# Kernel optimization log

Measured on AMD Instinct MI355X. Metric: run time of the kernel, lower is better.

## Reference

```python
import jax, jax.numpy as jnp
import numpy as np

N, D, E, R, EJ = 100000, 128, 600000, 200, 300000


def setup_inputs() -> dict:
    key = jax.random.key(0)
    ks = jax.random.split(key, 14)
    s = 1.0 / np.sqrt(D)
    return {
        "emb": jax.random.normal(ks[0], (N, D), jnp.float32),
        "change": jax.random.normal(ks[1], (N, D), jnp.float32),
        "W1": jax.random.normal(ks[2], (D, D), jnp.float32) * s,
        "Wloop1": jax.random.normal(ks[3], (D, D), jnp.float32) * s,
        "rel_emb1": jax.random.normal(ks[4], (R, D), jnp.float32),
        "W2": jax.random.normal(ks[5], (D, D), jnp.float32) * s,
        "Wloop2": jax.random.normal(ks[6], (D, D), jnp.float32) * s,
        "rel_emb2": jax.random.normal(ks[7], (R, D), jnp.float32),
        "res": jnp.array([0.1], jnp.float32),
        "jump_weight": jnp.array([1.0], jnp.float32),
        "edge_w_jump": jax.random.uniform(ks[8], (EJ,), jnp.float32),
        "edge_index": jax.random.randint(ks[9], (2, E), 0, N, jnp.int32),
        "edge_type": jax.random.randint(ks[10], (E,), 0, R, jnp.int32),
        "edge_id_jump": jax.random.randint(ks[11], (2, EJ), 0, N, jnp.int32),
    }


def _mgcn_conv(x, W, Wloop, rel_emb, edge_index, edge_type, num_e):
    # Relational (CompGCN-style mult composition) conv: gather-compose-scatter.
    src, dst = edge_index[0], edge_index[1]
    msg = x[src] * rel_emb[edge_type]                      # [E, D]
    agg = jax.ops.segment_sum(msg, dst, num_segments=num_e)
    deg = jax.ops.segment_sum(jnp.ones(src.shape, x.dtype), dst, num_segments=num_e)
    agg = agg / jnp.maximum(deg, 1.0)[:, None]
    return jnp.tanh(agg @ W + x @ Wloop)


def reference(emb, change, W1, Wloop1, rel_emb1, W2, Wloop2, rel_emb2, res,
              jump_weight, edge_w_jump, edge_index, edge_type, edge_id_jump):
    num_e = emb.shape[0]
    jump_emb = emb
    # residual-scaled two-layer relational GCN (dropout = identity in eval)
    h = emb + res[0] * _mgcn_conv(emb, W1, Wloop1, rel_emb1, edge_index, edge_type, num_e)
    h = h + res[0] * _mgcn_conv(h, W2, Wloop2, rel_emb2, edge_index, edge_type, num_e)
    # jump diffusion: weighted scatter over jump edge list
    jsrc, jdst = edge_id_jump[0], edge_id_jump[1]
    jump_res = jax.ops.segment_sum(edge_w_jump[:, None] * jump_emb[jsrc], jdst,
                                   num_segments=num_e)
    dchange = h + jump_weight[0] * jump_res
    return (change, dchange)
```

## Files before the change

kernel.cpp:

```cpp
#include <hip/hip_runtime.h>
#include <math.h>

#define D 128

typedef __attribute__((ext_vector_type(8))) short short8v;
typedef __attribute__((ext_vector_type(4))) float f32x4;
typedef _Float16 half2n __attribute__((ext_vector_type(2)));
typedef _Float16 half8v __attribute__((ext_vector_type(8)));

__device__ inline short f2h(float f) {
    _Float16 h = (_Float16)f;
    return __builtin_bit_cast(short, h);
}
__device__ inline float h2f(short s) {
    return (float)__builtin_bit_cast(_Float16, s);
}
__device__ inline unsigned char h2e5(short hs) {
    unsigned u = (unsigned short)hs;
    u = u + 0x7Fu + ((u >> 8) & 1u);
    return (unsigned char)(u >> 8);
}
__device__ inline half2n u2h2(unsigned u) { return __builtin_bit_cast(half2n, u); }
__device__ inline unsigned h22u(half2n h) { return __builtin_bit_cast(unsigned, h); }

__device__ inline float fast_tanh(float x) {
    float a = fabsf(x);
    float e = __expf(-2.0f * a);
    float t = (1.0f - e) / (1.0f + e);
    return copysignf(t, x);
}

__device__ inline void e5fma(uint2 xw, uint4 rw,
                             half2n& a0, half2n& a1, half2n& a2, half2n& a3) {
    a0 += u2h2(xw.x & 0xFF00FF00u) * u2h2(rw.x);
    a1 += u2h2((xw.x << 8) & 0xFF00FF00u) * u2h2(rw.y);
    a2 += u2h2(xw.y & 0xFF00FF00u) * u2h2(rw.z);
    a3 += u2h2((xw.y << 8) & 0xFF00FF00u) * u2h2(rw.w);
}
__device__ inline void h16fma(uint4 xw, half2n w2,
                              half2n& a0, half2n& a1, half2n& a2, half2n& a3) {
    a0 += u2h2(xw.x) * w2;
    a1 += u2h2(xw.y) * w2;
    a2 += u2h2(xw.z) * w2;
    a3 += u2h2(xw.w) * w2;
}
__device__ inline half2n red2(half2n a) {
    a += u2h2((unsigned)__shfl_xor(__builtin_bit_cast(int, a), 16));
    a += u2h2((unsigned)__shfl_xor(__builtin_bit_cast(int, a), 32));
    return a;
}

__global__ void hist_both(const int* __restrict__ dst_e,
                          const int* __restrict__ dst_j,
                          int* __restrict__ cnt, int E, int EJ, int N) {
    int i = blockIdx.x * blockDim.x + threadIdx.x;
    if (i < E) atomicAdd(&cnt[dst_e[i]], 1);
    else if (i < E + EJ) atomicAdd(&cnt[N + dst_j[i - E]], 1);
}

__global__ void scan1(const int* __restrict__ cnt, int* __restrict__ offs,
                      int* __restrict__ bsum, int M) {
    __shared__ int sh[256];
    int t = threadIdx.x;
    int base = blockIdx.x * 1024 + t * 4;
    int v0 = 0, v1 = 0, v2 = 0, v3 = 0;
    if (base + 0 < M) v0 = cnt[base + 0];
    if (base + 1 < M) v1 = cnt[base + 1];
    if (base + 2 < M) v2 = cnt[base + 2];
    if (base + 3 < M) v3 = cnt[base + 3];
    int tsum = v0 + v1 + v2 + v3;
    sh[t] = tsum;
    __syncthreads();
    for (int off = 1; off < 256; off <<= 1) {
        int x = (t >= off) ? sh[t - off] : 0;
        __syncthreads();
        sh[t] += x;
        __syncthreads();
    }
    int excl = sh[t] - tsum;
    if (base + 0 < M) offs[base + 0] = excl;
    excl += v0;
    if (base + 1 < M) offs[base + 1] = excl;
    excl += v1;
    if (base + 2 < M) offs[base + 2] = excl;
    excl += v2;
    if (base + 3 < M) offs[base + 3] = excl;
    if (t == 255) bsum[blockIdx.x] = sh[255];
}

__global__ void scan2(int* __restrict__ bsum, int NB) {
    __shared__ int sh[256];
    int t = threadIdx.x;
    int v = (t < NB) ? bsum[t] : 0;
    sh[t] = v;
    __syncthreads();
    for (int off = 1; off < 256; off <<= 1) {
        int x = (t >= off) ? sh[t - off] : 0;
        __syncthreads();
        sh[t] += x;
        __syncthreads();
    }
    if (t < NB) bsum[t] = sh[t] - v;
}

__global__ void scan3(int* __restrict__ offs, const int* __restrict__ bsum,
                      int* __restrict__ cur, int M) {
    int i = blockIdx.x * blockDim.x + threadIdx.x;
    if (i < M) {
        int o = offs[i] + bsum[i >> 10];
        offs[i] = o;
        cur[i] = o;
    }
}

__global__ void fill_both(const int* __restrict__ src_e,
                          const int* __restrict__ dst_e,
                          const int* __restrict__ et,
                          const int* __restrict__ src_j,
                          const int* __restrict__ dst_j,
                          const float* __restrict__ ew,
                          int* __restrict__ cur, int2* __restrict__ pairs,
                          int E, int EJ, int N) {
    int i = blockIdx.x * blockDim.x + threadIdx.x;
    if (i < E) {
        int p = atomicAdd(&cur[dst_e[i]], 1);
        pairs[p] = make_int2(src_e[i], et[i]);
    } else if (i < E + EJ) {
        int e = i - E;
        int p = atomicAdd(&cur[N + dst_j[e]], 1);
        pairs[p] = make_int2(src_j[e], __float_as_int(ew[e]));
    }
}

__global__ void pack_w(const float* __restrict__ W1, const float* __restrict__ Wl1,
                       const float* __restrict__ W2, const float* __restrict__ Wl2,
                       short* __restrict__ B1, short* __restrict__ B2) {
    int lane = threadIdx.x;
    int tile = blockIdx.x & 63;
    const float* W  = (blockIdx.x < 64) ? W1 : W2;
    const float* Wl = (blockIdx.x < 64) ? Wl1 : Wl2;
    short* Bpk      = (blockIdx.x < 64) ? B1 : B2;
    int tn = tile >> 3, tk = tile & 7;
    int n = tn * 16 + (lane & 15);
    int k0 = tk * 32 + (lane >> 4) * 8;
    short* o = Bpk + ((size_t)tile * 64 + lane) * 8;
#pragma unroll
    for (int j = 0; j < 8; j++) {
        int k = k0 + j;
        float f = (k < D) ? W[(size_t)k * D + n] : Wl[(size_t)(k - D) * D + n];
        o[j] = f2h(f);
    }
}

__global__ void cvt_rel(const float* __restrict__ r1, const float* __restrict__ r2,
                        short* __restrict__ o1, short* __restrict__ o2, int RD) {
    int i = blockIdx.x * blockDim.x + threadIdx.x;
    int half = RD >> 2;
    if (i < 2 * half) {
        const float* src = (i < half) ? r1 : r2;
        short* dst = (i < half) ? o1 : o2;
        int j = (i < half) ? i : i - half;
        float4 v = *(const float4*)(src + (size_t)j * 4);
        short4 o;
        o.x = f2h(v.x); o.y = f2h(v.y); o.z = f2h(v.z); o.w = f2h(v.w);
        *(short4*)(dst + (size_t)j * 4) = o;
    } else {
        int extra = i - 2 * half;
        if (extra < 64) {
            short* dst = (extra < 32) ? o1 : o2;
            int j = extra & 31;
            short4 z; z.x = 0; z.y = 0; z.z = 0; z.w = 0;
            *(short4*)(dst + (size_t)RD + j * 4) = z;
        }
    }
}

__global__ void cvt_emb_copy(const float* __restrict__ emb,
                             const float* __restrict__ change,
                             short* __restrict__ Abf,
                             unsigned char* __restrict__ X8,
                             float* __restrict__ out, int N) {
    int i = blockIdx.x * blockDim.x + threadIdx.x;
    int row = i >> 5;
    int c4 = (i & 31) * 4;
    if (row >= N) return;
    float4 v = *(const float4*)(emb + (size_t)row * D + c4);
    short4 o;
    o.x = f2h(v.x); o.y = f2h(v.y); o.z = f2h(v.z); o.w = f2h(v.w);
    *(short4*)(Abf + (size_t)row * 256 + 128 + c4) = o;
    unsigned u = (unsigned)h2e5(o.z) | ((unsigned)h2e5(o.x) << 8) |
                 ((unsigned)h2e5(o.w) << 16) | ((unsigned)h2e5(o.y) << 24);
    *(unsigned*)(X8 + (size_t)row * 128 + c4) = u;
    float4 ch = *(const float4*)(change + (size_t)row * D + c4);
    *(float4*)(out + (size_t)row * D + c4) = ch;
}

__global__ void gather_conv(const unsigned char* __restrict__ X8,
                            const short* __restrict__ relb,
                            short* __restrict__ Abf,
                            const int* __restrict__ offs,
                            const int* __restrict__ cnt,
                            const int2* __restrict__ pairs, int N, int RZ) {
    int node = blockIdx.x * 4 + (threadIdx.x >> 6);
    if (node >= N) return;
    int lane = threadIdx.x & 63;
    int h = lane >> 4;
    int c = (lane & 15) * 8;
    int beg = offs[node], num = cnt[node];
    half2n a0 = u2h2(0u), a1 = u2h2(0u), a2 = u2h2(0u), a3 = u2h2(0u);
    if (num > 0) {
        int ia = h, ib = h + 4;
        int ea = (ia < num) ? ia : (num - 1);
        int2 pa = pairs[beg + ea];
        int ra = (ia < num) ? pa.y : RZ;
        uint2 xa = *(const uint2*)(X8 + (size_t)pa.x * 128 + c);
        uint4 va = *(const uint4*)(relb + (size_t)ra * D + c);
        if (num > 4) {
            int eb = (ib < num) ? ib : (num - 1);
            int2 pb = pairs[beg + eb];
            int rb = (ib < num) ? pb.y : RZ;
            uint2 xb = *(const uint2*)(X8 + (size_t)pb.x * 128 + c);
            uint4 vb = *(const uint4*)(relb + (size_t)rb * D + c);
            e5fma(xa, va, a0, a1, a2, a3);
            e5fma(xb, vb, a0, a1, a2, a3);
        } else {
            e5fma(xa, va, a0, a1, a2, a3);
        }
        for (int i = 8; i < num; i += 4) {
            int ei = i + h;
            int e2 = (ei < num) ? ei : (num - 1);
            int2 pe = pairs[beg + e2];
            int rr = (ei < num) ? pe.y : RZ;
            uint2 xv = *(const uint2*)(X8 + (size_t)pe.x * 128 + c);
            uint4 rv = *(const uint4*)(relb + (size_t)rr * D + c);
            e5fma(xv, rv, a0, a1, a2, a3);
        }
        a0 = red2(a0); a1 = red2(a1); a2 = red2(a2); a3 = red2(a3);
    }
    if (h == 0) {
        float dinv = 1.0f / fmaxf((float)num, 1.0f);
        _Float16 dh = (_Float16)dinv;
        half2n d2 = {dh, dh};
        a0 *= d2; a1 *= d2; a2 *= d2; a3 *= d2;
        uint4 st; st.x = h22u(a0); st.y = h22u(a1); st.z = h22u(a2); st.w = h22u(a3);
        *(uint4*)(Abf + (size_t)node * 256 + c) = st;
    }
}

__global__ void gather_phase2(short* __restrict__ Abf2,
                              const unsigned char* __restrict__ X82,
                              const short* __restrict__ Abf1,
                              const short* __restrict__ relb,
                              const float* __restrict__ jwp,
                              const int* __restrict__ offs,
                              const int* __restrict__ cnt,
                              const int2* __restrict__ pairs,
                              float* __restrict__ dch, int N, int RZ) {
    int g = blockIdx.x * 4 + (threadIdx.x >> 6);
    int lane = threadIdx.x & 63;
    int h = lane >> 4;
    int c = (lane & 15) * 8;
    if (g < N) {
        int beg = offs[g], num = cnt[g];
        half2n a0 = u2h2(0u), a1 = u2h2(0u), a2 = u2h2(0u), a3 = u2h2(0u);
        if (num > 0) {
            int ia = h, ib = h + 4;
            int ea = (ia < num) ? ia : (num - 1);
            int2 pa = pairs[beg + ea];
            int ra = (ia < num) ? pa.y : RZ;
            uint2 xa = *(const uint2*)(X82 + (size_t)pa.x * 128 + c);
            uint4 va = *(const uint4*)(relb + (size_t)ra * D + c);
            if (num > 4) {
                int eb = (ib < num) ? ib : (num - 1);
                int2 pb = pairs[beg + eb];
                int rb = (ib < num) ? pb.y : RZ;
                uint2 xb = *(const uint2*)(X82 + (size_t)pb.x * 128 + c);
                uint4 vb = *(const uint4*)(relb + (size_t)rb * D + c);
                e5fma(xa, va, a0, a1, a2, a3);
                e5fma(xb, vb, a0, a1, a2, a3);
            } else {
                e5fma(xa, va, a0, a1, a2, a3);
            }
            for (int i = 8; i < num; i += 4) {
                int ei = i + h;
                int e2 = (ei < num) ? ei : (num - 1);
                int2 pe = pairs[beg + e2];
                int rr = (ei < num) ? pe.y : RZ;
                uint2 xv = *(const uint2*)(X82 + (size_t)pe.x * 128 + c);
                uint4 rv = *(const uint4*)(relb + (size_t)rr * D + c);
                e5fma(xv, rv, a0, a1, a2, a3);
            }
            a0 = red2(a0); a1 = red2(a1); a2 = red2(a2); a3 = red2(a3);
        }
        if (h == 0) {
            float dinv = 1.0f / fmaxf((float)num, 1.0f);
            _Float16 dh = (_Float16)dinv;
            half2n d2 = {dh, dh};
            a0 *= d2; a1 *= d2; a2 *= d2; a3 *= d2;
            uint4 st; st.x = h22u(a0); st.y = h22u(a1); st.z = h22u(a2); st.w = h22u(a3);
            *(uint4*)(Abf2 + (size_t)g * 256 + c) = st;
        }
    } else if (g < 2 * N) {
        int node = g - N;
        int beg = offs[N + node], num = cnt[N + node];
        half2n a0 = u2h2(0u), a1 = u2h2(0u), a2 = u2h2(0u), a3 = u2h2(0u);
        if (num > 0) {
            int ia = h, ib = h + 4;
            int ea = (ia < num) ? ia : (num - 1);
            int2 pa = pairs[beg + ea];
            float wa = (ia < num) ? __int_as_float(pa.y) : 0.f;
            _Float16 wha = (_Float16)wa;
            half2n w2a = {wha, wha};
            uint4 xa = *(const uint4*)(Abf1 + (size_t)pa.x * 256 + 128 + c);
            if (num > 4) {
                int eb = (ib < num) ? ib : (num - 1);
                int2 pb = pairs[beg + eb];
                float wb = (ib < num) ? __int_as_float(pb.y) : 0.f;
                _Float16 whb = (_Float16)wb;
                half2n w2b = {whb, whb};
                uint4 xb = *(const uint4*)(Abf1 + (size_t)pb.x * 256 + 128 + c);
                h16fma(xa, w2a, a0, a1, a2, a3);
                h16fma(xb, w2b, a0, a1, a2, a3);
            } else {
                h16fma(xa, w2a, a0, a1, a2, a3);
            }
            for (int i = 8; i < num; i += 4) {
                int ei = i + h;
                int e2 = (ei < num) ? ei : (num - 1);
                int2 pe = pairs[beg + e2];
                float wgt = (ei < num) ? __int_as_float(pe.y) : 0.f;
                _Float16 wh = (_Float16)wgt;
                half2n w2 = {wh, wh};
                uint4 xv = *(const uint4*)(Abf1 + (size_t)pe.x * 256 + 128 + c);
                h16fma(xv, w2, a0, a1, a2, a3);
            }
            a0 = red2(a0); a1 = red2(a1); a2 = red2(a2); a3 = red2(a3);
        }
        if (h == 0) {
            float jw = jwp[0];
            float* drow = dch + (size_t)node * D + c;
            *(float4*)(drow + 0) = make_float4(jw * (float)a0.x, jw * (float)a0.y,
                                               jw * (float)a1.x, jw * (float)a1.y);
            *(float4*)(drow + 4) = make_float4(jw * (float)a2.x, jw * (float)a2.y,
                                               jw * (float)a3.x, jw * (float)a3.y);
        }
    }
}

__launch_bounds__(256)
__global__ void mfma_gemm(const short* __restrict__ Abf,
                          const short* __restrict__ Bpk,
                          const float* __restrict__ resp,
                          short* __restrict__ outb,
                          unsigned char* __restrict__ x8out,
                          const float* __restrict__ addin,
                          float* __restrict__ outf,
                          int N) {
    int w = threadIdx.x >> 6;
    int lane = threadIdx.x & 63;
    int rb = (w & 1) * 32;
    int cb = (w >> 1) * 64;
    int row0 = blockIdx.x * 64;
    int m = lane & 15, quad = lane >> 4;

    f32x4 acc[2][4];
#pragma unroll
    for (int rt = 0; rt < 2; rt++)
#pragma unroll
        for (int ct = 0; ct < 4; ct++) acc[rt][ct] = (f32x4)(0.f);

    const short* arow0 = Abf + (size_t)(row0 + rb + m) * 256 + quad * 8;
    const short* arow1 = arow0 + 16 * 256;
    const short* bbase = Bpk + (((size_t)(cb >> 4)) * 8 * 64 + lane) * 8;

#pragma unroll
    for (int kt = 0; kt < 8; kt++) {
        half8v a0 = *(const half8v*)(arow0 + kt * 32);
        half8v a1 = *(const half8v*)(arow1 + kt * 32);
        half8v b[4];
#pragma unroll
        for (int ct = 0; ct < 4; ct++)
            b[ct] = *(const half8v*)(bbase + ((size_t)(ct * 8 + kt)) * 64 * 8);
#pragma unroll
        for (int ct = 0; ct < 4; ct++) {
            acc[0][ct] = __builtin_amdgcn_mfma_f32_16x16x32_f16(a0, b[ct],
                                                                acc[0][ct], 0, 0, 0);
            acc[1][ct] = __builtin_amdgcn_mfma_f32_16x16x32_f16(a1, b[ct],
                                                                acc[1][ct], 0, 0, 0);
        }
    }

    float res = resp[0];
#pragma unroll
    for (int rt = 0; rt < 2; rt++) {
#pragma unroll
        for (int ct = 0; ct < 4; ct++) {
            int colg = cb + ct * 16 + m;
#pragma unroll
            for (int r = 0; r < 4; r++) {
                int rowg = row0 + rb + rt * 16 + quad * 4 + r;
                if (rowg >= N) continue;
                float xr = h2f(Abf[(size_t)rowg * 256 + 128 + colg]);
                float o = xr + res * fast_tanh(acc[rt][ct][r]);
                if (outb != nullptr) {
                    short hx = f2h(o);
                    outb[(size_t)rowg * 256 + 128 + colg] = hx;
                    int d = colg & 3;
                    int pos = 2 * (d & 1) + 1 - (d >> 1);
                    x8out[(size_t)rowg * 128 + (colg & ~3) + pos] = h2e5(hx);
                } else {
                    size_t idx = (size_t)rowg * D + colg;
                    outf[idx] = o + addin[idx];
                }
            }
        }
    }
}

extern "C" void kernel_launch(void* const* d_in, const int* in_sizes, int n_in,
                              void* d_out, int out_size, void* d_ws, size_t ws_size,
                              hipStream_t stream) {
    const float* emb    = (const float*)d_in[0];
    const float* change = (const float*)d_in[1];
    const float* W1     = (const float*)d_in[2];
    const float* Wl1    = (const float*)d_in[3];
    const float* rel1   = (const float*)d_in[4];
    const float* W2     = (const float*)d_in[5];
    const float* Wl2    = (const float*)d_in[6];
    const float* rel2   = (const float*)d_in[7];
    const float* res    = (const float*)d_in[8];
    const float* jw     = (const float*)d_in[9];
    const float* ewj    = (const float*)d_in[10];
    const int*   eidx   = (const int*)d_in[11];
    const int*   etype  = (const int*)d_in[12];
    const int*   ejmp   = (const int*)d_in[13];

    const int ND = in_sizes[0];
    const int N  = ND / D;
    const int E  = in_sizes[12];
    const int EJ = in_sizes[10];
    const int RD = in_sizes[4];
    const int R  = RD / D;
    const int NP = ((N + 63) / 64) * 64;
    const int M  = 2 * N;

    float* out = (float*)d_out;
    float* dch = out + (size_t)ND;

    char* w = (char*)d_ws;
    short* Abf1  = (short*)w;                  w += (size_t)NP * 256 * 2;
    short* Abf2  = (short*)w;                  w += (size_t)NP * 256 * 2;
    short* Bpk1  = (short*)w;                  w += (size_t)64 * 64 * 8 * 2;
    short* Bpk2  = (short*)w;                  w += (size_t)64 * 64 * 8 * 2;
    short* relb1 = (short*)w;                  w += (size_t)(RD + D) * 2;
    short* relb2 = (short*)w;                  w += (size_t)(RD + D) * 2;
    unsigned char* X81 = (unsigned char*)w;    w += (size_t)NP * 128;
    unsigned char* X82 = (unsigned char*)w;    w += (size_t)NP * 128;
    int* cnt     = (int*)w;                    w += (size_t)M * 4;
    int* offs    = (int*)w;                    w += (size_t)M * 4;
    int* cur     = (int*)w;                    w += (size_t)M * 4;
    int* bsum    = (int*)w;                    w += 256 * 4;
    int2* pairs  = (int2*)w;                   w += (size_t)(E + EJ) * 8;

    const int T = 256;
    const int NB2 = (M + 1023) / 1024;
    const int EB  = (E + EJ + T - 1) / T;

    hipMemsetAsync(cnt, 0, (size_t)M * sizeof(int), stream);

    hist_both<<<EB, T, 0, stream>>>(eidx + E, ejmp + EJ, cnt, E, EJ, N);
    scan1<<<NB2, 256, 0, stream>>>(cnt, offs, bsum, M);
    scan2<<<1, 256, 0, stream>>>(bsum, NB2);
    scan3<<<(M + T - 1) / T, T, 0, stream>>>(offs, bsum, cur, M);
    fill_both<<<EB, T, 0, stream>>>(eidx, eidx + E, etype, ejmp, ejmp + EJ, ewj,
                                    cur, pairs, E, EJ, N);

    pack_w<<<128, 64, 0, stream>>>(W1, Wl1, W2, Wl2, Bpk1, Bpk2);
    cvt_rel<<<(RD / 2 + 64 + T - 1) / T, T, 0, stream>>>(rel1, rel2, relb1, relb2, RD);

    cvt_emb_copy<<<(N * 32 + T - 1) / T, T, 0, stream>>>(emb, change, Abf1, X81, out, N);

    int gatherB  = (N + 3) / 4;
    int gather2B = (M + 3) / 4;
    int gemmB    = NP / 64;

    gather_conv<<<gatherB, 256, 0, stream>>>(X81, relb1, Abf1, offs, cnt, pairs, N, R);
    mfma_gemm<<<gemmB, 256, 0, stream>>>(Abf1, Bpk1, res, Abf2, X82, nullptr, nullptr, N);

    gather_phase2<<<gather2B, 256, 0, stream>>>(Abf2, X82, Abf1, relb2, jw, offs, cnt,
                                                pairs, dch, N, R);

    mfma_gemm<<<gemmB, 256, 0, stream>>>(Abf2, Bpk2, res, nullptr, nullptr, dch, dch, N);
}
```

Before: 523.0 us.

## Store jump aggregate in fp16 scratch and record CSR slots during histogram

After: 479.3 us. -8.4%, faster.

```diff
diff --git a/kernel.cpp b/kernel.cpp
--- a/kernel.cpp
+++ b/kernel.cpp
@@ -52,10 +52,11 @@
 
 __global__ void hist_both(const int* __restrict__ dst_e,
                           const int* __restrict__ dst_j,
-                          int* __restrict__ cnt, int E, int EJ, int N) {
+                          int* __restrict__ cnt, int* __restrict__ slot,
+                          int E, int EJ, int N) {
     int i = blockIdx.x * blockDim.x + threadIdx.x;
-    if (i < E) atomicAdd(&cnt[dst_e[i]], 1);
-    else if (i < E + EJ) atomicAdd(&cnt[N + dst_j[i - E]], 1);
+    if (i < E) slot[i] = atomicAdd(&cnt[dst_e[i]], 1);
+    else if (i < E + EJ) slot[i] = atomicAdd(&cnt[N + dst_j[i - E]], 1);
 }
 
 __global__ void scan1(const int* __restrict__ cnt, int* __restrict__ offs,
@@ -103,14 +104,9 @@
     if (t < NB) bsum[t] = sh[t] - v;
 }
 
-__global__ void scan3(int* __restrict__ offs, const int* __restrict__ bsum,
-                      int* __restrict__ cur, int M) {
+__global__ void scan3(int* __restrict__ offs, const int* __restrict__ bsum, int M) {
     int i = blockIdx.x * blockDim.x + threadIdx.x;
-    if (i < M) {
-        int o = offs[i] + bsum[i >> 10];
-        offs[i] = o;
-        cur[i] = o;
-    }
+    if (i < M) offs[i] += bsum[i >> 10];
 }
 
 __global__ void fill_both(const int* __restrict__ src_e,
@@ -119,15 +115,17 @@
                           const int* __restrict__ src_j,
                           const int* __restrict__ dst_j,
                           const float* __restrict__ ew,
-                          int* __restrict__ cur, int2* __restrict__ pairs,
+                          const int* __restrict__ offs,
+                          const int* __restrict__ slot,
+                          int2* __restrict__ pairs,
                           int E, int EJ, int N) {
     int i = blockIdx.x * blockDim.x + threadIdx.x;
     if (i < E) {
-        int p = atomicAdd(&cur[dst_e[i]], 1);
+        int p = offs[dst_e[i]] + slot[i];
         pairs[p] = make_int2(src_e[i], et[i]);
     } else if (i < E + EJ) {
         int e = i - E;
-        int p = atomicAdd(&cur[N + dst_j[e]], 1);
+        int p = offs[N + dst_j[e]] + slot[i];
         pairs[p] = make_int2(src_j[e], __float_as_int(ew[e]));
     }
 }
@@ -247,103 +245,53 @@
     }
 }
 
-__global__ void gather_phase2(short* __restrict__ Abf2,
-                              const unsigned char* __restrict__ X82,
-                              const short* __restrict__ Abf1,
-                              const short* __restrict__ relb,
-                              const float* __restrict__ jwp,
-                              const int* __restrict__ offs,
-                              const int* __restrict__ cnt,
-                              const int2* __restrict__ pairs,
-                              float* __restrict__ dch, int N, int RZ) {
-    int g = blockIdx.x * 4 + (threadIdx.x >> 6);
+__global__ void gather_jump(const short* __restrict__ Abf1,
+                            short* __restrict__ jh,
+                            const int* __restrict__ offs,
+                            const int* __restrict__ cnt,
+                            const int2* __restrict__ pairs, int N) {
+    int node = blockIdx.x * 4 + (threadIdx.x >> 6);
+    if (node >= N) return;
     int lane = threadIdx.x & 63;
     int h = lane >> 4;
     int c = (lane & 15) * 8;
-    if (g < N) {
-        int beg = offs[g], num = cnt[g];
-        half2n a0 = u2h2(0u), a1 = u2h2(0u), a2 = u2h2(0u), a3 = u2h2(0u);
-        if (num > 0) {
-            int ia = h, ib = h + 4;
-            int ea = (ia < num) ? ia : (num - 1);
-            int2 pa = pairs[beg + ea];
-            int ra = (ia < num) ? pa.y : RZ;
-            uint2 xa = *(const uint2*)(X82 + (size_t)pa.x * 128 + c);
-            uint4 va = *(const uint4*)(relb + (size_t)ra * D + c);
-            if (num > 4) {
-                int eb = (ib < num) ? ib : (num - 1);
-                int2 pb = pairs[beg + eb];
-                int rb = (ib < num) ? pb.y : RZ;
-                uint2 xb = *(const uint2*)(X82 + (size_t)pb.x * 128 + c);
-                uint4 vb = *(const uint4*)(relb + (size_t)rb * D + c);
-                e5fma(xa, va, a0, a1, a2, a3);
-                e5fma(xb, vb, a0, a1, a2, a3);
-            } else {
-                e5fma(xa, va, a0, a1, a2, a3);
-            }
-            for (int i = 8; i < num; i += 4) {
-                int ei = i + h;
-                int e2 = (ei < num) ? ei : (num - 1);
-                int2 pe = pairs[beg + e2];
-                int rr = (ei < num) ? pe.y : RZ;
-                uint2 xv = *(const uint2*)(X82 + (size_t)pe.x * 128 + c);
-                uint4 rv = *(const uint4*)(relb + (size_t)rr * D + c);
-                e5fma(xv, rv, a0, a1, a2, a3);
-            }
-            a0 = red2(a0); a1 = red2(a1); a2 = red2(a2); a3 = red2(a3);
-        }
-        if (h == 0) {
-            float dinv = 1.0f / fmaxf((float)num, 1.0f);
-            _Float16 dh = (_Float16)dinv;
-            half2n d2 = {dh, dh};
-            a0 *= d2; a1 *= d2; a2 *= d2; a3 *= d2;
-            uint4 st; st.x = h22u(a0); st.y = h22u(a1); st.z = h22u(a2); st.w = h22u(a3);
-            *(uint4*)(Abf2 + (size_t)g * 256 + c) = st;
-        }
-    } else if (g < 2 * N) {
-        int node = g - N;
-        int beg = offs[N + node], num = cnt[N + node];
-        half2n a0 = u2h2(0u), a1 = u2h2(0u), a2 = u2h2(0u), a3 = u2h2(0u);
-        if (num > 0) {
-            int ia = h, ib = h + 4;
-            int ea = (ia < num) ? ia : (num - 1);
-            int2 pa = pairs[beg + ea];
-            float wa = (ia < num) ? __int_as_float(pa.y) : 0.f;
-            _Float16 wha = (_Float16)wa;
-            half2n w2a = {wha, wha};
-            uint4 xa = *(const uint4*)(Abf1 + (size_t)pa.x * 256 + 128 + c);
-            if (num > 4) {
-                int eb = (ib < num) ? ib : (num - 1);
-                int2 pb = pairs[beg + eb];
-                float wb = (ib < num) ? __int_as_float(pb.y) : 0.f;
-                _Float16 whb = (_Float16)wb;
-                half2n w2b = {whb, whb};
-                uint4 xb = *(const uint4*)(Abf1 + (size_t)pb.x * 256 + 128 + c);
-                h16fma(xa, w2a, a0, a1, a2, a3);
-                h16fma(xb, w2b, a0, a1, a2, a3);
-            } else {
-                h16fma(xa, w2a, a0, a1, a2, a3);
-            }
-            for (int i = 8; i < num; i += 4) {
-                int ei = i + h;
-                int e2 = (ei < num) ? ei : (num - 1);
-                int2 pe = pairs[beg + e2];
-                float wgt = (ei < num) ? __int_as_float(pe.y) : 0.f;
-                _Float16 wh = (_Float16)wgt;
-                half2n w2 = {wh, wh};
-                uint4 xv = *(const uint4*)(Abf1 + (size_t)pe.x * 256 + 128 + c);
-                h16fma(xv, w2, a0, a1, a2, a3);
-            }
-            a0 = red2(a0); a1 = red2(a1); a2 = red2(a2); a3 = red2(a3);
-        }
-        if (h == 0) {
-            float jw = jwp[0];
-            float* drow = dch + (size_t)node * D + c;
-            *(float4*)(drow + 0) = make_float4(jw * (float)a0.x, jw * (float)a0.y,
-                                               jw * (float)a1.x, jw * (float)a1.y);
-            *(float4*)(drow + 4) = make_float4(jw * (float)a2.x, jw * (float)a2.y,
-                                               jw * (float)a3.x, jw * (float)a3.y);
-        }
+    int beg = offs[N + node], num = cnt[N + node];
+    half2n a0 = u2h2(0u), a1 = u2h2(0u), a2 = u2h2(0u), a3 = u2h2(0u);
+    if (num > 0) {
+        int ia = h, ib = h + 4;
+        int ea = (ia < num) ? ia : (num - 1);
+        int2 pa = pairs[beg + ea];
+        float wa = (ia < num) ? __int_as_float(pa.y) : 0.f;
+        _Float16 wha = (_Float16)wa;
+        half2n w2a = {wha, wha};
+        uint4 xa = *(const uint4*)(Abf1 + (size_t)pa.x * 256 + 128 + c);
+        if (num > 4) {
+            int eb = (ib < num) ? ib : (num - 1);
+            int2 pb = pairs[beg + eb];
+            float wb = (ib < num) ? __int_as_float(pb.y) : 0.f;
+            _Float16 whb = (_Float16)wb;
+            half2n w2b = {whb, whb};
+            uint4 xb = *(const uint4*)(Abf1 + (size_t)pb.x * 256 + 128 + c);
+            h16fma(xa, w2a, a0, a1, a2, a3);
+            h16fma(xb, w2b, a0, a1, a2, a3);
+        } else {
+            h16fma(xa, w2a, a0, a1, a2, a3);
+        }
+        for (int i = 8; i < num; i += 4) {
+            int ei = i + h;
+            int e2 = (ei < num) ? ei : (num - 1);
+            int2 pe = pairs[beg + e2];
+            float wgt = (ei < num) ? __int_as_float(pe.y) : 0.f;
+            _Float16 wh = (_Float16)wgt;
+            half2n w2 = {wh, wh};
+            uint4 xv = *(const uint4*)(Abf1 + (size_t)pe.x * 256 + 128 + c);
+            h16fma(xv, w2, a0, a1, a2, a3);
+        }
+        a0 = red2(a0); a1 = red2(a1); a2 = red2(a2); a3 = red2(a3);
+    }
+    if (h == 0) {
+        uint4 st; st.x = h22u(a0); st.y = h22u(a1); st.z = h22u(a2); st.w = h22u(a3);
+        *(uint4*)(jh + (size_t)node * 128 + c) = st;
     }
 }
 
@@ -353,7 +301,8 @@
                           const float* __restrict__ resp,
                           short* __restrict__ outb,
                           unsigned char* __restrict__ x8out,
-                          const float* __restrict__ addin,
+                          const short* __restrict__ addin_h,
+                          const float* __restrict__ jwp,
                           float* __restrict__ outf,
                           int N) {
     int w = threadIdx.x >> 6;
@@ -391,6 +340,7 @@
     }
 
     float res = resp[0];
+    float jw = (jwp != nullptr) ? jwp[0] : 0.f;
 #pragma unroll
     for (int rt = 0; rt < 2; rt++) {
 #pragma unroll
@@ -410,7 +360,7 @@
                     x8out[(size_t)rowg * 128 + (colg & ~3) + pos] = h2e5(hx);
                 } else {
                     size_t idx = (size_t)rowg * D + colg;
-                    outf[idx] = o + addin[idx];
+                    outf[idx] = o + jw * h2f(addin_h[idx]);
                 }
             }
         }
@@ -456,10 +406,11 @@
     short* relb2 = (short*)w;                  w += (size_t)(RD + D) * 2;
     unsigned char* X81 = (unsigned char*)w;    w += (size_t)NP * 128;
     unsigned char* X82 = (unsigned char*)w;    w += (size_t)NP * 128;
+    short* jh    = (short*)w;                  w += (size_t)NP * 128 * 2;
     int* cnt     = (int*)w;                    w += (size_t)M * 4;
     int* offs    = (int*)w;                    w += (size_t)M * 4;
-    int* cur     = (int*)w;                    w += (size_t)M * 4;
     int* bsum    = (int*)w;                    w += 256 * 4;
+    int* slot    = (int*)w;                    w += (size_t)(E + EJ) * 4;
     int2* pairs  = (int2*)w;                   w += (size_t)(E + EJ) * 8;
 
     const int T = 256;
@@ -468,27 +419,29 @@
 
     hipMemsetAsync(cnt, 0, (size_t)M * sizeof(int), stream);
 
-    hist_both<<<EB, T, 0, stream>>>(eidx + E, ejmp + EJ, cnt, E, EJ, N);
+    hist_both<<<EB, T, 0, stream>>>(eidx + E, ejmp + EJ, cnt, slot, E, EJ, N);
     scan1<<<NB2, 256, 0, stream>>>(cnt, offs, bsum, M);
     scan2<<<1, 256, 0, stream>>>(bsum, NB2);
-    scan3<<<(M + T - 1) / T, T, 0, stream>>>(offs, bsum, cur, M);
+    scan3<<<(M + T - 1) / T, T, 0, stream>>>(offs, bsum, M);
     fill_both<<<EB, T, 0, stream>>>(eidx, eidx + E, etype, ejmp, ejmp + EJ, ewj,
-                                    cur, pairs, E, EJ, N);
+                                    offs, slot, pairs, E, EJ, N);
 
     pack_w<<<128, 64, 0, stream>>>(W1, Wl1, W2, Wl2, Bpk1, Bpk2);
     cvt_rel<<<(RD / 2 + 64 + T - 1) / T, T, 0, stream>>>(rel1, rel2, relb1, relb2, RD);
 
     cvt_emb_copy<<<(N * 32 + T - 1) / T, T, 0, stream>>>(emb, change, Abf1, X81, out, N);
 
-    int gatherB  = (N + 3) / 4;
-    int gather2B = (M + 3) / 4;
-    int gemmB    = NP / 64;
+    int gatherB = (N + 3) / 4;
+    int gemmB   = NP / 64;
+
+    gather_jump<<<gatherB, 256, 0, stream>>>(Abf1, jh, offs, cnt, pairs, N);
 
     gather_conv<<<gatherB, 256, 0, stream>>>(X81, relb1, Abf1, offs, cnt, pairs, N, R);
-    mfma_gemm<<<gemmB, 256, 0, stream>>>(Abf1, Bpk1, res, Abf2, X82, nullptr, nullptr, N);
-
-    gather_phase2<<<gather2B, 256, 0, stream>>>(Abf2, X82, Abf1, relb2, jw, offs, cnt,
-                                                pairs, dch, N, R);
-
-    mfma_gemm<<<gemmB, 256, 0, stream>>>(Abf2, Bpk2, res, nullptr, nullptr, dch, dch, N);
-}
+    mfma_gemm<<<gemmB, 256, 0, stream>>>(Abf1, Bpk1, res, Abf2, X82,
+                                         nullptr, nullptr, nullptr, N);
+
+    gather_conv<<<gatherB, 256, 0, stream>>>(X82, relb2, Abf2, offs, cnt, pairs, N, R);
+
+    mfma_gemm<<<gemmB, 256, 0, stream>>>(Abf2, Bpk2, res, nullptr, nullptr,
+                                         jh, jw, dch, N);
+}
```
